# Kernel tuning notes

Hardware: AMD Instinct MI355X
Metric: run time of the kernel (lower is better)

## Reference

```python
import jax, jax.numpy as jnp
import numpy as np

T, B, L, I, H = 1024, 1024, 10, 10, 10


def setup_inputs() -> dict:
    key = jax.random.key(0)
    ks = jax.random.split(key, 7)
    scale = 1.0 / np.sqrt(H)
    x = jax.random.normal(ks[0], (T, B, I), dtype=jnp.float32)
    hp = jax.random.normal(ks[1], (L, B, H), dtype=jnp.float32)
    cp = jax.random.normal(ks[2], (L, B, H), dtype=jnp.float32)
    # torch nn.LSTM params, uniform(-1/sqrt(H), 1/sqrt(H)); layer 0 input = I == H so all layers stack
    W_ih = jax.random.uniform(ks[3], (L, 4 * H, I), minval=-scale, maxval=scale, dtype=jnp.float32)
    W_hh = jax.random.uniform(ks[4], (L, 4 * H, H), minval=-scale, maxval=scale, dtype=jnp.float32)
    b_ih = jax.random.uniform(ks[5], (L, 4 * H), minval=-scale, maxval=scale, dtype=jnp.float32)
    b_hh = jax.random.uniform(ks[6], (L, 4 * H), minval=-scale, maxval=scale, dtype=jnp.float32)
    return {"x": x, "hp": hp, "cp": cp, "W_ih": W_ih, "W_hh": W_hh, "b_ih": b_ih, "b_hh": b_hh}


def _run_layer(inp, h0, c0, Wi, Wh, bi, bh):
    # precompute input projections for all timesteps: [T, B, 4H]
    xg = jnp.einsum('tbi,gi->tbg', inp, Wi) + bi + bh

    def step(carry, xg_t):
        h, c = carry
        g = xg_t + h @ Wh.T  # [B, 4H]; torch gate order: i, f, g, o
        i_g, f_g, g_g, o_g = jnp.split(g, 4, axis=-1)
        i_g = jax.nn.sigmoid(i_g)
        f_g = jax.nn.sigmoid(f_g)
        g_g = jnp.tanh(g_g)
        o_g = jax.nn.sigmoid(o_g)
        c = f_g * c + i_g * g_g
        h = o_g * jnp.tanh(c)
        return (h, c), h

    (hT, cT), ys = jax.lax.scan(step, (h0, c0), xg)
    return ys, hT, cT


def reference(x, hp, cp, W_ih, W_hh, b_ih, b_hh):
    out = x
    hns, cns = [], []
    for l in range(hp.shape[0]):  # fixed small layer stack
        out, hn, cn = _run_layer(out, hp[l], cp[l], W_ih[l], W_hh[l], b_ih[l], b_hh[l])
        hns.append(hn)
        cns.append(cn)
    return out, jnp.stack(hns), jnp.stack(cns)
```

## Files before the change

### kernel.cpp

```cpp
#include <hip/hip_runtime.h>

namespace {

constexpr int T = 1024;
constexpr int B = 1024;
constexpr int L = 10;
constexpr int H = 10;
constexpr int NTHREADS = 128;
constexpr int U = 4;
constexpr int NWIN = T / U;
constexpr int NINT = NWIN + L - 1;
constexpr int BH = B * H;
constexpr int ROWF = 20;
constexpr int P = 4;
constexpr int DELAY = P - 1;
constexpr int D = 2 * P;
constexpr int NROUNDS = ((NINT + DELAY + P - 1) / P) * P;

using v2f = __attribute__((ext_vector_type(2))) float;
using v4f = __attribute__((ext_vector_type(4))) float;

__device__ __forceinline__ v2f v2fma(v2f a, v2f b, v2f c) {
    return __builtin_elementwise_fma(a, b, c);
}
__device__ __forceinline__ void pin2(v2f& v) { asm volatile("" : "+v"(v)); }
__device__ __forceinline__ float rcp_f(float x) { return __builtin_amdgcn_rcpf(x); }
__device__ __forceinline__ v2f lo2(v4f q) { return __builtin_shufflevector(q, q, 0, 1); }
__device__ __forceinline__ v2f hi2(v4f q) { return __builtin_shufflevector(q, q, 2, 3); }

__global__
__attribute__((amdgpu_flat_work_group_size(NTHREADS, NTHREADS)))
__attribute__((amdgpu_waves_per_eu(2)))
void lstm_pipeline(const float* __restrict__ x,
                   const float* __restrict__ hp,
                   const float* __restrict__ cp,
                   const float* __restrict__ Wih,
                   const float* __restrict__ Whh,
                   const float* __restrict__ bih,
                   const float* __restrict__ bhh,
                   float* __restrict__ out,
                   float* __restrict__ hn,
                   float* __restrict__ cn)
{
    __shared__ __align__(16) float buf[D][U][L + 1][ROWF];

    const int tid = threadIdx.x;
    const int wv = tid >> 6;
    const int ln = tid & 63;
    int lidx;
    if (wv == 0) lidx = (ln < 60) ? ln : (ln - 10);
    else         lidx = (ln < 40) ? (60 + ln) : (90 + (ln - 40) % 10);
    const int l = lidx / 10;
    const int j = lidx % 10;
    const int b = blockIdx.x;
    const int boff = b * H + j;

    v2f wiA[10], wiB[10], whA[10], whB[10], bA, bB;
    {
        const float* WiL = Wih + (size_t)l * 4 * H * H;
        const float* WhL = Whh + (size_t)l * 4 * H * H;
        #pragma unroll
        for (int k = 0; k < 10; ++k) {
            wiA[k][0] = WiL[(0 * H + j) * H + k]; wiA[k][1] = WiL[(1 * H + j) * H + k];
            wiB[k][0] = WiL[(2 * H + j) * H + k]; wiB[k][1] = WiL[(3 * H + j) * H + k];
            whA[k][0] = WhL[(0 * H + j) * H + k]; whA[k][1] = WhL[(1 * H + j) * H + k];
            whB[k][0] = WhL[(2 * H + j) * H + k]; whB[k][1] = WhL[(3 * H + j) * H + k];
        }
        const int bo = l * 4 * H;
        bA[0] = bih[bo + j] + bhh[bo + j];
        bA[1] = bih[bo + H + j] + bhh[bo + H + j];
        bB[0] = bih[bo + 2 * H + j] + bhh[bo + 2 * H + j];
        bB[1] = bih[bo + 3 * H + j] + bhh[bo + 3 * H + j];
    }
    #pragma unroll
    for (int k = 0; k < 10; ++k) { pin2(wiA[k]); pin2(wiB[k]); pin2(whA[k]); pin2(whB[k]); }
    pin2(bA); pin2(bB);

    float h = hp[(l * B + b) * H + j];
    float c = cp[(l * B + b) * H + j];
    {
        const int ss = (unsigned)(l - 1 + D) & (D - 1);
        v2f hh; hh[0] = h; hh[1] = h;
        *(v2f*)&buf[ss][U - 1][l + 1][2 * j] = hh;
    }

    const bool is_st = (lidx < 10);
    float xcur[U], xnext[U];
    if (is_st) {
        #pragma unroll
        for (int u = 0; u < U; ++u) {
            float xv = x[(size_t)u * BH + boff];
            v2f xx; xx[0] = xv; xx[1] = xv;
            *(v2f*)&buf[D - 1][u][0][2 * j] = xx;
        }
        #pragma unroll
        for (int u = 0; u < U; ++u) xcur[u] = x[(size_t)(U + u) * BH + boff];
    }
    __syncthreads();

    auto interval = [&](int k) {
        const int slot_w = (unsigned)(k + 2 * D) & (D - 1);
        const int slot_r = (unsigned)(k - 1 + 2 * D) & (D - 1);
        if (is_st && (k + 2) < NWIN) {
            #pragma unroll
            for (int u = 0; u < U; ++u)
                xnext[u] = x[(size_t)((k + 2) * U + u) * BH + boff];
        }
        const unsigned w = (unsigned)(k - l);
        if (w < (unsigned)NWIN) {
            v2f aA[U], aB[U];
            #pragma unroll
            for (int u = 0; u < U; ++u) {
                const float* xr = &buf[slot_r][u][l][0];
                v4f q0 = *(const v4f*)(xr + 0);
                v4f q1 = *(const v4f*)(xr + 4);
                v4f q2 = *(const v4f*)(xr + 8);
                v4f q3 = *(const v4f*)(xr + 12);
                v4f q4 = *(const v4f*)(xr + 16);
                v2f a1 = v2fma(wiA[0], lo2(q0), bA);
                v2f a2 = wiA[1] * hi2(q0);
                v2f b1 = v2fma(wiB[0], lo2(q0), bB);
                v2f b2 = wiB[1] * hi2(q0);
                a1 = v2fma(wiA[2], lo2(q1), a1);  a2 = v2fma(wiA[3], hi2(q1), a2);
                b1 = v2fma(wiB[2], lo2(q1), b1);  b2 = v2fma(wiB[3], hi2(q1), b2);
                a1 = v2fma(wiA[4], lo2(q2), a1);  a2 = v2fma(wiA[5], hi2(q2), a2);
                b1 = v2fma(wiB[4], lo2(q2), b1);  b2 = v2fma(wiB[5], hi2(q2), b2);
                a1 = v2fma(wiA[6], lo2(q3), a1);  a2 = v2fma(wiA[7], hi2(q3), a2);
                b1 = v2fma(wiB[6], lo2(q3), b1);  b2 = v2fma(wiB[7], hi2(q3), b2);
                a1 = v2fma(wiA[8], lo2(q4), a1);  a2 = v2fma(wiA[9], hi2(q4), a2);
                b1 = v2fma(wiB[8], lo2(q4), b1);  b2 = v2fma(wiB[9], hi2(q4), b2);
                aA[u] = a1 + a2;
                aB[u] = b1 + b2;
            }
            float hv[U];
            #pragma unroll
            for (int u = 0; u < U; ++u) {
                const float* hr = (u == 0) ? &buf[slot_r][U - 1][l + 1][0]
                                           : &buf[slot_w][u - 1][l + 1][0];
                v4f q0 = *(const v4f*)(hr + 0);
                v4f q1 = *(const v4f*)(hr + 4);
                v4f q2 = *(const v4f*)(hr + 8);
                v4f q3 = *(const v4f*)(hr + 12);
                v4f q4 = *(const v4f*)(hr + 16);
                v2f a1 = v2fma(whA[0], lo2(q0), aA[u]);
                v2f a2 = whA[1] * hi2(q0);
                v2f b1 = v2fma(whB[0], lo2(q0), aB[u]);
                v2f b2 = whB[1] * hi2(q0);
                a1 = v2fma(whA[2], lo2(q1), a1);  a2 = v2fma(whA[3], hi2(q1), a2);
                b1 = v2fma(whB[2], lo2(q1), b1);  b2 = v2fma(whB[3], hi2(q1), b2);
                a1 = v2fma(whA[4], lo2(q2), a1);  a2 = v2fma(whA[5], hi2(q2), a2);
                b1 = v2fma(whB[4], lo2(q2), b1);  b2 = v2fma(whB[5], hi2(q2), b2);
                a1 = v2fma(whA[6], lo2(q3), a1);  a2 = v2fma(whA[7], hi2(q3), a2);
                b1 = v2fma(whB[6], lo2(q3), b1);  b2 = v2fma(whB[7], hi2(q3), b2);
                a1 = v2fma(whA[8], lo2(q4), a1);  a2 = v2fma(whA[9], hi2(q4), a2);
                b1 = v2fma(whB[8], lo2(q4), b1);  b2 = v2fma(whB[9], hi2(q4), b2);
                const v2f pA = a1 + a2;
                const v2f pB = b1 + b2;
                const float ei = __expf(-pA[0]);
                const float ef = __expf(-pA[1]);
                const float eg = __expf(2.0f * pB[0]);
                const float eo = __expf(-pB[1]);
                const float ig = rcp_f(1.0f + ei);
                const float fg = rcp_f(1.0f + ef);
                const float gr = rcp_f(1.0f + eg);
                const float og = rcp_f(1.0f + eo);
                const float gg = 1.0f - 2.0f * gr;
                c = fmaf(fg, c, ig * gg);
                const float th = 1.0f - 2.0f * rcp_f(1.0f + __expf(2.0f * c));
                h = og * th;
                v2f hh; hh[0] = h; hh[1] = h;
                *(v2f*)&buf[slot_w][u][l + 1][2 * j] = hh;
                hv[u] = h;
            }
            if (l == L - 1) {
                const int t0 = (int)w * U;
                #pragma unroll
                for (int u = 0; u < U; ++u)
                    out[(size_t)(t0 + u) * BH + boff] = hv[u];
            }
        }
        if (is_st && (k + 1) < NWIN) {
            #pragma unroll
            for (int u = 0; u < U; ++u) {
                v2f xx; xx[0] = xcur[u]; xx[1] = xcur[u];
                *(v2f*)&buf[slot_w][u][0][2 * j] = xx;
            }
            #pragma unroll
            for (int u = 0; u < U; ++u) xcur[u] = xnext[u];
        }
    };

    for (int rr = 0; rr < NROUNDS; rr += P) {
        #pragma unroll
        for (int pp = 0; pp < P; ++pp) {
            const int k = (rr + pp) - (wv ? DELAY : 0);
            interval(k);
            asm volatile("" ::: "memory");
        }
        __syncthreads();
    }

    hn[(l * B + b) * H + j] = h;
    cn[(l * B + b) * H + j] = c;
}

}

extern "C" void kernel_launch(void* const* d_in, const int* in_sizes, int n_in,
                              void* d_out, int out_size, void* d_ws, size_t ws_size,
                              hipStream_t stream) {
    (void)in_sizes; (void)n_in; (void)d_ws; (void)ws_size; (void)out_size;
    const float* x   = (const float*)d_in[0];
    const float* hp  = (const float*)d_in[1];
    const float* cp  = (const float*)d_in[2];
    const float* Wih = (const float*)d_in[3];
    const float* Whh = (const float*)d_in[4];
    const float* bih = (const float*)d_in[5];
    const float* bhh = (const float*)d_in[6];

    float* out = (float*)d_out;
    float* hn  = out + (size_t)T * B * H;
    float* cn  = hn + (size_t)L * B * H;

    lstm_pipeline<<<dim3(B), dim3(NTHREADS), 0, stream>>>(
        x, hp, cp, Wih, Whh, bih, bhh, out, hn, cn);
}
```

Measured before the change: 537.5 us.

## Sync every interval with double buffer and fold exp scaling into weights

Replaces the skewed two-wave schedule (wave 1 delayed by P-1 intervals, an 8-slot LDS ring, one barrier per P intervals) with a plain 2-slot double buffer and a barrier after every interval. Pre-multiplies the weights and biases by -log2(e), or -2·log2(e) for the cell gate, so the gate nonlinearities use raw v_exp_f32. The gate math is also regrouped to need fewer reciprocals by merging denominators. This trades more frequent barriers for less LDS and fewer transcendental ops; the merged denominators could overflow or lose precision for large pre-activations.

```diff
diff --git a/kernel.cpp b/kernel.cpp
--- a/kernel.cpp
+++ b/kernel.cpp
@@ -12,10 +12,6 @@
 constexpr int NINT = NWIN + L - 1;
 constexpr int BH = B * H;
 constexpr int ROWF = 20;
-constexpr int P = 4;
-constexpr int DELAY = P - 1;
-constexpr int D = 2 * P;
-constexpr int NROUNDS = ((NINT + DELAY + P - 1) / P) * P;
 
 using v2f = __attribute__((ext_vector_type(2))) float;
 using v4f = __attribute__((ext_vector_type(4))) float;
@@ -25,6 +21,9 @@
 }
 __device__ __forceinline__ void pin2(v2f& v) { asm volatile("" : "+v"(v)); }
 __device__ __forceinline__ float rcp_f(float x) { return __builtin_amdgcn_rcpf(x); }
+__device__ __forceinline__ float exp2_f(float x) {
+    float r; asm("v_exp_f32 %0, %1" : "=v"(r) : "v"(x)); return r;
+}
 __device__ __forceinline__ v2f lo2(v4f q) { return __builtin_shufflevector(q, q, 0, 1); }
 __device__ __forceinline__ v2f hi2(v4f q) { return __builtin_shufflevector(q, q, 2, 3); }
 
@@ -42,7 +41,7 @@
                    float* __restrict__ hn,
                    float* __restrict__ cn)
 {
-    __shared__ __align__(16) float buf[D][U][L + 1][ROWF];
+    __shared__ __align__(16) float buf[2][U][L + 1][ROWF];
 
     const int tid = threadIdx.x;
     const int wv = tid >> 6;
@@ -55,22 +54,32 @@
     const int b = blockIdx.x;
     const int boff = b * H + j;
 
+    const float NL2E = -1.44269504088896340736f;
+    v2f sA; sA[0] = NL2E;        sA[1] = NL2E;
+    v2f sB; sB[0] = 2.0f * NL2E; sB[1] = NL2E;
     v2f wiA[10], wiB[10], whA[10], whB[10], bA, bB;
     {
         const float* WiL = Wih + (size_t)l * 4 * H * H;
         const float* WhL = Whh + (size_t)l * 4 * H * H;
         #pragma unroll
         for (int k = 0; k < 10; ++k) {
-            wiA[k][0] = WiL[(0 * H + j) * H + k]; wiA[k][1] = WiL[(1 * H + j) * H + k];
-            wiB[k][0] = WiL[(2 * H + j) * H + k]; wiB[k][1] = WiL[(3 * H + j) * H + k];
-            whA[k][0] = WhL[(0 * H + j) * H + k]; whA[k][1] = WhL[(1 * H + j) * H + k];
-            whB[k][0] = WhL[(2 * H + j) * H + k]; whB[k][1] = WhL[(3 * H + j) * H + k];
+            v2f t;
+            t[0] = WiL[(0 * H + j) * H + k]; t[1] = WiL[(1 * H + j) * H + k];
+            wiA[k] = t * sA;
+            t[0] = WiL[(2 * H + j) * H + k]; t[1] = WiL[(3 * H + j) * H + k];
+            wiB[k] = t * sB;
+            t[0] = WhL[(0 * H + j) * H + k]; t[1] = WhL[(1 * H + j) * H + k];
+            whA[k] = t * sA;
+            t[0] = WhL[(2 * H + j) * H + k]; t[1] = WhL[(3 * H + j) * H + k];
+            whB[k] = t * sB;
         }
         const int bo = l * 4 * H;
         bA[0] = bih[bo + j] + bhh[bo + j];
         bA[1] = bih[bo + H + j] + bhh[bo + H + j];
         bB[0] = bih[bo + 2 * H + j] + bhh[bo + 2 * H + j];
         bB[1] = bih[bo + 3 * H + j] + bhh[bo + 3 * H + j];
+        bA = bA * sA;
+        bB = bB * sB;
     }
     #pragma unroll
     for (int k = 0; k < 10; ++k) { pin2(wiA[k]); pin2(wiB[k]); pin2(whA[k]); pin2(whB[k]); }
@@ -79,9 +88,8 @@
     float h = hp[(l * B + b) * H + j];
     float c = cp[(l * B + b) * H + j];
     {
-        const int ss = (unsigned)(l - 1 + D) & (D - 1);
         v2f hh; hh[0] = h; hh[1] = h;
-        *(v2f*)&buf[ss][U - 1][l + 1][2 * j] = hh;
+        *(v2f*)&buf[(l + 1) & 1][U - 1][l + 1][2 * j] = hh;
     }
 
     const bool is_st = (lidx < 10);
@@ -91,16 +99,14 @@
         for (int u = 0; u < U; ++u) {
             float xv = x[(size_t)u * BH + boff];
             v2f xx; xx[0] = xv; xx[1] = xv;
-            *(v2f*)&buf[D - 1][u][0][2 * j] = xx;
+            *(v2f*)&buf[1][u][0][2 * j] = xx;
         }
         #pragma unroll
         for (int u = 0; u < U; ++u) xcur[u] = x[(size_t)(U + u) * BH + boff];
     }
     __syncthreads();
 
-    auto interval = [&](int k) {
-        const int slot_w = (unsigned)(k + 2 * D) & (D - 1);
-        const int slot_r = (unsigned)(k - 1 + 2 * D) & (D - 1);
+    auto interval = [&](int k, int wp, int rp) {
         if (is_st && (k + 2) < NWIN) {
             #pragma unroll
             for (int u = 0; u < U; ++u)
@@ -108,10 +114,15 @@
         }
         const unsigned w = (unsigned)(k - l);
         if (w < (unsigned)NWIN) {
+            v4f hq0 = *(const v4f*)&buf[rp][U - 1][l + 1][0];
+            v4f hq1 = *(const v4f*)&buf[rp][U - 1][l + 1][4];
+            v4f hq2 = *(const v4f*)&buf[rp][U - 1][l + 1][8];
+            v4f hq3 = *(const v4f*)&buf[rp][U - 1][l + 1][12];
+            v4f hq4 = *(const v4f*)&buf[rp][U - 1][l + 1][16];
             v2f aA[U], aB[U];
             #pragma unroll
             for (int u = 0; u < U; ++u) {
-                const float* xr = &buf[slot_r][u][l][0];
+                const float* xr = &buf[rp][u][l][0];
                 v4f q0 = *(const v4f*)(xr + 0);
                 v4f q1 = *(const v4f*)(xr + 4);
                 v4f q2 = *(const v4f*)(xr + 8);
@@ -135,13 +146,16 @@
             float hv[U];
             #pragma unroll
             for (int u = 0; u < U; ++u) {
-                const float* hr = (u == 0) ? &buf[slot_r][U - 1][l + 1][0]
-                                           : &buf[slot_w][u - 1][l + 1][0];
-                v4f q0 = *(const v4f*)(hr + 0);
-                v4f q1 = *(const v4f*)(hr + 4);
-                v4f q2 = *(const v4f*)(hr + 8);
-                v4f q3 = *(const v4f*)(hr + 12);
-                v4f q4 = *(const v4f*)(hr + 16);
+                v4f q0, q1, q2, q3, q4;
+                if (u == 0) { q0 = hq0; q1 = hq1; q2 = hq2; q3 = hq3; q4 = hq4; }
+                else {
+                    const float* hr = &buf[wp][u - 1][l + 1][0];
+                    q0 = *(const v4f*)(hr + 0);
+                    q1 = *(const v4f*)(hr + 4);
+                    q2 = *(const v4f*)(hr + 8);
+                    q3 = *(const v4f*)(hr + 12);
+                    q4 = *(const v4f*)(hr + 16);
+                }
                 v2f a1 = v2fma(whA[0], lo2(q0), aA[u]);
                 v2f a2 = whA[1] * hi2(q0);
                 v2f b1 = v2fma(whB[0], lo2(q0), aB[u]);
@@ -156,20 +170,22 @@
                 b1 = v2fma(whB[8], lo2(q4), b1);  b2 = v2fma(whB[9], hi2(q4), b2);
                 const v2f pA = a1 + a2;
                 const v2f pB = b1 + b2;
-                const float ei = __expf(-pA[0]);
-                const float ef = __expf(-pA[1]);
-                const float eg = __expf(2.0f * pB[0]);
-                const float eo = __expf(-pB[1]);
-                const float ig = rcp_f(1.0f + ei);
-                const float fg = rcp_f(1.0f + ef);
-                const float gr = rcp_f(1.0f + eg);
-                const float og = rcp_f(1.0f + eo);
-                const float gg = 1.0f - 2.0f * gr;
-                c = fmaf(fg, c, ig * gg);
-                const float th = 1.0f - 2.0f * rcp_f(1.0f + __expf(2.0f * c));
-                h = og * th;
+                const float Ei = exp2_f(pA[0]);
+                const float Ef = exp2_f(pA[1]);
+                const float Eg = exp2_f(pB[0]);
+                const float Eo = exp2_f(pB[1]);
+                const float d1 = 1.0f + Ef;
+                const float e1 = 1.0f + Ei;
+                const float e2 = 1.0f + Eg;
+                const float d2 = e1 * e2;
+                const float num = fmaf(c, d2, (1.0f - Eg) * d1);
+                c = num * rcp_f(d1 * d2);
+                const float Ec = exp2_f((2.0f * NL2E) * c);
+                const float o1 = 1.0f + Eo;
+                const float o2 = 1.0f + Ec;
+                h = (1.0f - Ec) * rcp_f(o1 * o2);
                 v2f hh; hh[0] = h; hh[1] = h;
-                *(v2f*)&buf[slot_w][u][l + 1][2 * j] = hh;
+                *(v2f*)&buf[wp][u][l + 1][2 * j] = hh;
                 hv[u] = h;
             }
             if (l == L - 1) {
@@ -183,21 +199,17 @@
             #pragma unroll
             for (int u = 0; u < U; ++u) {
                 v2f xx; xx[0] = xcur[u]; xx[1] = xcur[u];
-                *(v2f*)&buf[slot_w][u][0][2 * j] = xx;
+                *(v2f*)&buf[wp][u][0][2 * j] = xx;
             }
             #pragma unroll
             for (int u = 0; u < U; ++u) xcur[u] = xnext[u];
         }
+        __syncthreads();
     };
 
-    for (int rr = 0; rr < NROUNDS; rr += P) {
-        #pragma unroll
-        for (int pp = 0; pp < P; ++pp) {
-            const int k = (rr + pp) - (wv ? DELAY : 0);
-            interval(k);
-            asm volatile("" ::: "memory");
-        }
-        __syncthreads();
+    for (int kk = 0; kk < NINT + 1; kk += 2) {
+        interval(kk, 0, 1);
+        interval(kk + 1, 1, 0);
     }
 
     hn[(l * B + b) * H + j] = h;
```

Result: faster. 488.0 us (-9.2%).
